# Kernel optimization log

Hardware: AMD Instinct MI355X
Metric: run time of the kernel (lower is better)

## Reference

```python
import jax, jax.numpy as jnp
import numpy as np

B, S, H = 2, 2048, 2048
NH, NKV, D = 16, 4, 128
E, K, F = 16, 2, 768
EPS = 1e-6
THETA = 1e6


def setup_inputs() -> dict:
    key = jax.random.key(0)
    ks = jax.random.split(key, 10)
    sd = 0.02
    rn = lambda k, shp: jax.random.normal(k, shp, jnp.float32) * sd
    return {
        "positions": jnp.arange(S, dtype=jnp.int32),
        "hidden_states": jax.random.normal(ks[0], (B, S, H), jnp.float32),
        "residual": jax.random.normal(ks[1], (B, S, H), jnp.float32),
        "w_in_ln": jnp.ones((H,), jnp.float32),
        "wq": rn(ks[2], (H, NH * D)),
        "wk": rn(ks[3], (H, NKV * D)),
        "wv": rn(ks[4], (H, NKV * D)),
        "wo": rn(ks[5], (NH * D, H)),
        "q_norm_w": jnp.ones((D,), jnp.float32),
        "k_norm_w": jnp.ones((D,), jnp.float32),
        "w_post_ln": jnp.ones((H,), jnp.float32),
        "gate_w": rn(ks[6], (H, E)),
        "w_gate_up": rn(ks[7], (E, H, 2 * F)),
        "w_down": rn(ks[8], (E, F, H)),
    }


def _rmsnorm(x, w):
    return x * jax.lax.rsqrt(jnp.mean(x * x, axis=-1, keepdims=True) + EPS) * w


def _rope(x, positions):
    # x: [B, S, h, D], neox-style rotate-half RoPE
    half = D // 2
    inv_freq = 1.0 / (THETA ** (jnp.arange(half, dtype=jnp.float32) / half))
    ang = positions.astype(jnp.float32)[:, None] * inv_freq  # [S, half]
    cos = jnp.cos(ang)[None, :, None, :]
    sin = jnp.sin(ang)[None, :, None, :]
    x1, x2 = x[..., :half], x[..., half:]
    return jnp.concatenate([x1 * cos - x2 * sin, x2 * cos + x1 * sin], axis=-1)


def reference(positions, hidden_states, residual, w_in_ln, wq, wk, wv, wo,
              q_norm_w, k_norm_w, w_post_ln, gate_w, w_gate_up, w_down):
    # fused RMSNorm + residual (residual is not None branch)
    residual = hidden_states + residual
    h = _rmsnorm(residual, w_in_ln)

    # --- Qwen3 attention: qk-norm + RoPE + causal GQA ---
    q = _rmsnorm((h @ wq).reshape(B, S, NH, D), q_norm_w)
    k = _rmsnorm((h @ wk).reshape(B, S, NKV, D), k_norm_w)
    v = (h @ wv).reshape(B, S, NKV, D)
    q = _rope(q, positions)
    k = _rope(k, positions)
    rep = NH // NKV
    k = jnp.repeat(k, rep, axis=2)
    v = jnp.repeat(v, rep, axis=2)
    scores = jnp.einsum('bqhd,bkhd->bhqk', q, k) / np.sqrt(D).astype(np.float32)
    causal = jnp.tril(jnp.ones((S, S), bool))
    scores = jnp.where(causal, scores, -jnp.inf)
    attn = jax.nn.softmax(scores, axis=-1)
    o = jnp.einsum('bhqk,bkhd->bqhd', attn, v).reshape(B, S, NH * D) @ wo

    # fused RMSNorm + residual
    residual = o + residual
    h = _rmsnorm(residual, w_post_ln)

    # --- MoE: top-k router (renormalized) + capacity-based grouped GEMM dispatch ---
    x = h.reshape(-1, H)                      # [T, H]
    T = B * S
    probs = jax.nn.softmax((x @ gate_w).astype(jnp.float32), axis=-1)
    tw, tids = jax.lax.top_k(probs, K)        # [T, K]
    tw = (tw / tw.sum(axis=-1, keepdims=True)).astype(x.dtype)

    P = T * K
    C = (2 * P) // E
    eids = tids.reshape(-1)                   # [P]
    oneh = jax.nn.one_hot(eids, E, dtype=jnp.int32)
    pos_in_e = (jnp.cumsum(oneh, axis=0) * oneh).sum(-1) - 1   # slot within expert
    valid = pos_in_e < C
    pos_c = jnp.minimum(pos_in_e, C - 1)
    e_safe = jnp.where(valid, eids, E)        # overflow -> dump row E

    xr = jnp.repeat(x, K, axis=0)             # [P, H]
    buf = jnp.zeros((E + 1, C, H), x.dtype).at[e_safe, pos_c].set(xr)[:E]
    gu = jnp.einsum('ech,ehf->ecf', buf, w_gate_up)            # [E, C, 2F]
    g, u = jnp.split(gu, 2, axis=-1)
    dn = jnp.einsum('ecf,efh->ech', jax.nn.silu(g) * u, w_down)
    dn = jnp.concatenate([dn, jnp.zeros((1, C, H), dn.dtype)], axis=0)
    yp = dn[e_safe, pos_c] * tw.reshape(-1)[:, None]           # [P, H]
    y = yp.reshape(T, K, H).sum(axis=1)
    return y.reshape(B, S, H), residual
```

## Files before the change

kernel.cpp:

```cpp
#include <hip/hip_runtime.h>
#include <stdint.h>

#define T_TOK 4096
#define HDIM  2048
#define SEQ   2048
#define NHQ   16
#define NKVH  4
#define DH    128
#define NE    16
#define CCAP  1024
#define FF    768
#define EPSF  1e-6f

typedef __attribute__((ext_vector_type(4))) float          f32x4;
typedef __attribute__((ext_vector_type(8))) _Float16       f16x8;
typedef __attribute__((ext_vector_type(4))) unsigned short u16x4;
typedef __attribute__((ext_vector_type(8))) unsigned short u16x8;

__device__ __forceinline__ unsigned short f2h(float f){ return __builtin_bit_cast(unsigned short, (_Float16)f); }
__device__ __forceinline__ float h2f(unsigned short u){ return (float)__builtin_bit_cast(_Float16, u); }
__device__ __forceinline__ void split2(float x, unsigned short& hi, unsigned short& lo){
  unsigned short h = f2h(x);
  hi = h; lo = f2h((x - h2f(h)) * 4096.f);
}
__device__ __forceinline__ void gl_lds16(const void* g, void* l){
  __builtin_amdgcn_global_load_lds((const __attribute__((address_space(1))) unsigned int*)g,
                                   (__attribute__((address_space(3))) unsigned int*)l, 16, 0, 0);
}
__device__ __forceinline__ int bswz(int row){ return ((row & 7) ^ ((row >> 3) & 7)) << 3; }

__global__ __launch_bounds__(256) void k_addnorm(
    const float* __restrict__ hs, const float* __restrict__ rs, const float* __restrict__ w,
    float* __restrict__ resid, unsigned short* __restrict__ hhi, unsigned short* __restrict__ hlo)
{
  int t = blockIdx.x, tid = threadIdx.x;
  size_t off = (size_t)t * HDIM;
  float4 a0 = ((const float4*)(hs+off))[tid];
  float4 b0 = ((const float4*)(rs+off))[tid];
  float4 a1 = ((const float4*)(hs+off))[tid+256];
  float4 b1 = ((const float4*)(rs+off))[tid+256];
  float4 s0 = make_float4(a0.x+b0.x, a0.y+b0.y, a0.z+b0.z, a0.w+b0.w);
  float4 s1 = make_float4(a1.x+b1.x, a1.y+b1.y, a1.z+b1.z, a1.w+b1.w);
  float ssq = s0.x*s0.x+s0.y*s0.y+s0.z*s0.z+s0.w*s0.w
            + s1.x*s1.x+s1.y*s1.y+s1.z*s1.z+s1.w*s1.w;
  #pragma unroll
  for (int sh=1; sh<64; sh<<=1) ssq += __shfl_xor(ssq, sh);
  __shared__ float red[4];
  if ((tid & 63) == 0) red[tid>>6] = ssq;
  __syncthreads();
  float tot = red[0]+red[1]+red[2]+red[3];
  float r = 1.f / sqrtf(tot * (1.f/HDIM) + EPSF);
  ((float4*)(resid+off))[tid]     = s0;
  ((float4*)(resid+off))[tid+256] = s1;
  float4 w0 = ((const float4*)w)[tid];
  float4 w1 = ((const float4*)w)[tid+256];
  u16x4 hv, lv; unsigned short ta, tb;
  split2(s0.x*r*w0.x, ta, tb); hv.x=ta; lv.x=tb;
  split2(s0.y*r*w0.y, ta, tb); hv.y=ta; lv.y=tb;
  split2(s0.z*r*w0.z, ta, tb); hv.z=ta; lv.z=tb;
  split2(s0.w*r*w0.w, ta, tb); hv.w=ta; lv.w=tb;
  ((u16x4*)(hhi+off))[tid] = hv; ((u16x4*)(hlo+off))[tid] = lv;
  split2(s1.x*r*w1.x, ta, tb); hv.x=ta; lv.x=tb;
  split2(s1.y*r*w1.y, ta, tb); hv.y=ta; lv.y=tb;
  split2(s1.z*r*w1.z, ta, tb); hv.z=ta; lv.z=tb;
  split2(s1.w*r*w1.w, ta, tb); hv.w=ta; lv.w=tb;
  ((u16x4*)(hhi+off))[tid+256] = hv; ((u16x4*)(hlo+off))[tid+256] = lv;
}

__global__ void k_cstab(const int* __restrict__ pos, float* __restrict__ cs)
{
  int i = blockIdx.x*256 + threadIdx.x;
  if (i >= SEQ*64) return;
  int s = i >> 6, f = i & 63;
  float pw  = (float)exp((double)f * 13.815510557964274 / 64.0);
  float inv = 1.0f / pw;
  float ang = (float)pos[s] * inv;
  float sv, cv;
  sincosf(ang, &sv, &cv);
  ((float2*)cs)[i] = make_float2(cv, sv);
}

__global__ __launch_bounds__(256) void k_normrope(
    unsigned short* __restrict__ qh, unsigned short* __restrict__ ql,
    unsigned short* __restrict__ kh, unsigned short* __restrict__ kl,
    const float* __restrict__ qnw, const float* __restrict__ knw,
    const float* __restrict__ cs)
{
  int t = blockIdx.x, head = blockIdx.y*4 + (threadIdx.x>>6), lane = threadIdx.x & 63;
  int s = t & (SEQ-1);
  unsigned short *dh, *dl; const float* wn; float scale; size_t off;
  if (head < NHQ){ off = ((size_t)t*NHQ + head)*DH; dh = qh+off; dl = ql+off; wn = qnw; scale = 0.08838834764831845f; }
  else           { off = ((size_t)t*NKVH + (head-NHQ))*DH; dh = kh+off; dl = kl+off; wn = knw; scale = 1.f; }
  float x1 = h2f(dh[lane])    + h2f(dl[lane])   *(1.f/4096.f);
  float x2 = h2f(dh[lane+64]) + h2f(dl[lane+64])*(1.f/4096.f);
  float ssq = x1*x1 + x2*x2;
  #pragma unroll
  for (int sh=1; sh<64; sh<<=1) ssq += __shfl_xor(ssq, sh);
  float r = 1.f / sqrtf(ssq * (1.f/DH) + EPSF);
  float y1 = x1*r*wn[lane], y2 = x2*r*wn[lane+64];
  float2 csp = ((const float2*)cs)[s*64 + lane];
  float o1 = (y1*csp.x - y2*csp.y) * scale;
  float o2 = (y2*csp.x + y1*csp.y) * scale;
  unsigned short a, b;
  split2(o1, a, b); dh[lane]    = a; dl[lane]    = b;
  split2(o2, a, b); dh[lane+64] = a; dl[lane+64] = b;
}

__global__ __launch_bounds__(256) void k_wsplit(
    const float* __restrict__ W, int Kd, int Ncols,
    unsigned short* __restrict__ Whi, unsigned short* __restrict__ Wlo)
{
  int k0 = blockIdx.x*64, n0 = blockIdx.y*64;
  __shared__ float T[64][65];
  int tid = threadIdx.x;
  int tr = tid >> 4;
  int tc = (tid & 15) * 4;
  #pragma unroll
  for (int i=0;i<4;i++){
    int k = tr + i*16;
    float4 v = *(const float4*)(W + (size_t)(k0 + k)*Ncols + n0 + tc);
    T[k][tc+0]=v.x; T[k][tc+1]=v.y; T[k][tc+2]=v.z; T[k][tc+3]=v.w;
  }
  __syncthreads();
  int n  = tid >> 2;
  int kc = (tid & 3) * 16;
  u16x8 hv0, lv0, hv1, lv1;
  #pragma unroll
  for (int j=0;j<8;j++){
    unsigned short hi, lo; split2(T[kc+j][n], hi, lo);
    hv0[j]=hi; lv0[j]=lo;
  }
  #pragma unroll
  for (int j=0;j<8;j++){
    unsigned short hi, lo; split2(T[kc+8+j][n], hi, lo);
    hv1[j]=hi; lv1[j]=lo;
  }
  size_t ob = (size_t)(n0 + n)*Kd + k0 + kc;
  *(u16x8*)(Whi + ob)     = hv0;
  *(u16x8*)(Whi + ob + 8) = hv1;
  *(u16x8*)(Wlo + ob)     = lv0;
  *(u16x8*)(Wlo + ob + 8) = lv1;
}

__global__ __launch_bounds__(256,2) void k_gemm_qkv(
    const unsigned short* __restrict__ Ahi, const unsigned short* __restrict__ Alo,
    const unsigned short* __restrict__ Whi, const unsigned short* __restrict__ Wlo,
    unsigned short* __restrict__ qh, unsigned short* __restrict__ ql,
    unsigned short* __restrict__ kh, unsigned short* __restrict__ kl,
    unsigned short* __restrict__ vh, unsigned short* __restrict__ vl)
{
  const int Kd = HDIM;
  int bm = blockIdx.x, bn2 = blockIdx.y;
  int bn, N, noff; unsigned short *Ch, *Cl;
  if (bn2 < 16){ bn = bn2;      N = 2048; noff = 0;    Ch = qh; Cl = ql; }
  else if (bn2 < 20){ bn = bn2-16; N = 512; noff = 2048; Ch = kh; Cl = kl; }
  else { bn = bn2-20; N = 512; noff = 2560; Ch = vh; Cl = vl; }

  __shared__ unsigned short As[2][8192];
  __shared__ unsigned short Bs[2][8192];

  int tid = threadIdx.x, lane = tid & 63, w = tid >> 6;
  int wr = w >> 1, wc = w & 1;

  size_t arow_g[4], brow_g[4];
  int lb_[4];
  #pragma unroll
  for (int i=0;i<4;i++){
    int ob = w*4096 + i*1024 + lane*16;
    int row = ob >> 7;
    int colB = ob & 127;
    int scolB = colB ^ ((row & 7) << 4);
    arow_g[i] = (size_t)(bm*128 + row) * Kd + (scolB >> 1);
    brow_g[i] = (size_t)(noff + bn*128 + row) * Kd + (scolB >> 1);
    lb_[i] = (w*4096 + i*1024) >> 1;
  }

  f32x4 accA[4][4] = {};
  f32x4 accB[4][4] = {};

  for (int kt = 0; kt < Kd/64; kt++){
    #pragma unroll
    for (int i=0;i<4;i++){
      gl_lds16(Ahi + arow_g[i] + kt*64, (void*)&As[0][lb_[i]]);
      gl_lds16(Alo + arow_g[i] + kt*64, (void*)&As[1][lb_[i]]);
      gl_lds16(Whi + brow_g[i] + kt*64, (void*)&Bs[0][lb_[i]]);
      gl_lds16(Wlo + brow_g[i] + kt*64, (void*)&Bs[1][lb_[i]]);
    }
    __syncthreads();
    #pragma unroll
    for (int kk=0; kk<2; kk++){
      f16x8 ah[4], al[4], bh[4], bl[4];
      #pragma unroll
      for (int m=0;m<4;m++){
        int row = wr*64 + m*16 + (lane & 15);
        int ci = (kk*32 + ((lane>>4)<<3)) ^ ((row & 7) << 3);
        ah[m] = *(const f16x8*)&As[0][row*64 + ci];
        al[m] = *(const f16x8*)&As[1][row*64 + ci];
      }
      #pragma unroll
      for (int n=0;n<4;n++){
        int row = wc*64 + n*16 + (lane & 15);
        int ci = (kk*32 + ((lane>>4)<<3)) ^ ((row & 7) << 3);
        bh[n] = *(const f16x8*)&Bs[0][row*64 + ci];
        bl[n] = *(const f16x8*)&Bs[1][row*64 + ci];
      }
      #pragma unroll
      for (int m=0;m<4;m++)
        #pragma unroll
        for (int n=0;n<4;n++){
          accA[m][n] = __builtin_amdgcn_mfma_f32_16x16x32_f16(ah[m], bh[n], accA[m][n], 0,0,0);
          accB[m][n] = __builtin_amdgcn_mfma_f32_16x16x32_f16(ah[m], bl[n], accB[m][n], 0,0,0);
          accB[m][n] = __builtin_amdgcn_mfma_f32_16x16x32_f16(al[m], bh[n], accB[m][n], 0,0,0);
        }
    }
    __syncthreads();
  }
  int r0 = (lane >> 4) << 2, c0 = lane & 15;
  #pragma unroll
  for (int m=0;m<4;m++){
    int grow0 = bm*128 + wr*64 + m*16 + r0;
    #pragma unroll
    for (int n=0;n<4;n++){
      int gcol = bn*128 + wc*64 + n*16 + c0;
      #pragma unroll
      for (int j=0;j<4;j++){
        float v = accA[m][n][j] + accB[m][n][j] * (1.f/4096.f);
        int grow = grow0 + j;
        unsigned short hi, lo; split2(v, hi, lo);
        Ch[(size_t)grow*N + gcol] = hi;
        Cl[(size_t)grow*N + gcol] = lo;
      }
    }
  }
}

template<int MODE>
__global__ __launch_bounds__(256,2) void k_gemm(
    const unsigned short* __restrict__ Ahi, const unsigned short* __restrict__ Alo,
    const float* __restrict__ Bsrc,
    const unsigned short* __restrict__ Bhi, const unsigned short* __restrict__ Blo,
    void* __restrict__ C1,
    int N, int Kd,
    const int* __restrict__ erow, const int* __restrict__ counts,
    const float* __restrict__ topw)
{
  constexpr int SPLIT = (MODE <= 2) ? 1 : 0;
  int bm = blockIdx.x, bn = blockIdx.y, e = blockIdx.z;
  int cnt = 0;
  const unsigned short* Abase = Ahi;
  const float* Bp = Bsrc;
  if constexpr (MODE == 4){ cnt = counts[e]; if (bm*128 >= cnt) return; Bp = Bsrc + (size_t)e*Kd*N; Abase = Ahi + (size_t)e*CCAP*Kd; }

  __shared__ unsigned short As[SPLIT?2:1][8192];
  __shared__ unsigned short Bs[SPLIT?2:1][8192];

  int tid = threadIdx.x, lane = tid & 63, w = tid >> 6;
  int wr = w >> 1, wc = w & 1;

  size_t arow_g[4], brow_g[4];
  int lb_[4];
  #pragma unroll
  for (int i=0;i<4;i++){
    int ob = w*4096 + i*1024 + lane*16;
    int row = ob >> 7;
    int colB = ob & 127;
    int scolB = colB ^ ((row & 7) << 4);
    int grow = bm*128 + row;
    arow_g[i] = (size_t)grow * Kd + (scolB >> 1);
    brow_g[i] = (size_t)(bn*128 + row) * Kd + (scolB >> 1);
    lb_[i] = (w*4096 + i*1024) >> 1;
  }

  f32x4 accA[4][4] = {};
  f32x4 accB[4][4] = {};

  int nK = Kd >> 6;
  for (int kt = 0; kt < nK; kt++){
    #pragma unroll
    for (int i=0;i<4;i++){
      gl_lds16(Abase + arow_g[i] + kt*64, (void*)&As[0][lb_[i]]);
      if constexpr (SPLIT) gl_lds16(Alo + arow_g[i] + kt*64, (void*)&As[1][lb_[i]]);
    }
    if constexpr (SPLIT){
      #pragma unroll
      for (int i=0;i<4;i++){
        gl_lds16(Bhi + brow_g[i] + kt*64, (void*)&Bs[0][lb_[i]]);
        gl_lds16(Blo + brow_g[i] + kt*64, (void*)&Bs[1][lb_[i]]);
      }
    } else {
      #pragma unroll
      for (int it=0; it<2; it++){
        int b2 = tid + it*256;
        int k0 = (b2 >> 5) << 2;
        int n0 = (b2 & 31) << 2;
        const float* bp = Bp + (size_t)(kt*64 + k0)*N + bn*128 + n0;
        float4 f0 = *(const float4*)bp;
        float4 f1 = *(const float4*)(bp + (size_t)N);
        float4 f2 = *(const float4*)(bp + 2*(size_t)N);
        float4 f3 = *(const float4*)(bp + 3*(size_t)N);
        #define DO_COL(J, CX) { \
          int rown = n0 + J; \
          int idx = rown*64 + (k0 ^ bswz(rown)); \
          u16x4 ph; ph.x=f2h(f0.CX); ph.y=f2h(f1.CX); ph.z=f2h(f2.CX); ph.w=f2h(f3.CX); \
          *(u16x4*)&Bs[0][idx] = ph; }
        DO_COL(0, x) DO_COL(1, y) DO_COL(2, z) DO_COL(3, w)
        #undef DO_COL
      }
    }
    __syncthreads();
    #pragma unroll
    for (int kk=0; kk<2; kk++){
      f16x8 ah[4], al[4], bh[4], bl[4];
      #pragma unroll
      for (int m=0;m<4;m++){
        int row = wr*64 + m*16 + (lane & 15);
        int ci = (kk*32 + ((lane>>4)<<3)) ^ ((row & 7) << 3);
        ah[m] = *(const f16x8*)&As[0][row*64 + ci];
        if constexpr (SPLIT) al[m] = *(const f16x8*)&As[1][row*64 + ci];
      }
      #pragma unroll
      for (int n=0;n<4;n++){
        int row = wc*64 + n*16 + (lane & 15);
        int sw = SPLIT ? ((row & 7) << 3) : bswz(row);
        int ci = (kk*32 + ((lane>>4)<<3)) ^ sw;
        bh[n] = *(const f16x8*)&Bs[0][row*64 + ci];
        if constexpr (SPLIT) bl[n] = *(const f16x8*)&Bs[1][row*64 + ci];
      }
      #pragma unroll
      for (int m=0;m<4;m++)
        #pragma unroll
        for (int n=0;n<4;n++){
          accA[m][n] = __builtin_amdgcn_mfma_f32_16x16x32_f16(ah[m], bh[n], accA[m][n], 0,0,0);
          if constexpr (SPLIT){
            accB[m][n] = __builtin_amdgcn_mfma_f32_16x16x32_f16(ah[m], bl[n], accB[m][n], 0,0,0);
            accB[m][n] = __builtin_amdgcn_mfma_f32_16x16x32_f16(al[m], bh[n], accB[m][n], 0,0,0);
          }
        }
    }
    __syncthreads();
  }
  int r0 = (lane >> 4) << 2, c0 = lane & 15;
  #pragma unroll
  for (int m=0;m<4;m++){
    int grow0 = bm*128 + wr*64 + m*16 + r0;
    #pragma unroll
    for (int n=0;n<4;n++){
      int gcol = bn*128 + wc*64 + n*16 + c0;
      #pragma unroll
      for (int j=0;j<4;j++){
        float v = accA[m][n][j];
        if constexpr (SPLIT) v += accB[m][n][j] * (1.f/4096.f);
        int grow = grow0 + j;
        if constexpr (MODE == 2){
          size_t idx = (size_t)grow*N + gcol;
          ((float*)C1)[idx] += v;
        } else if constexpr (MODE == 4){
          if (grow < cnt){
            int p = erow[e*CCAP + grow];
            ((float*)C1)[(size_t)p*N + gcol] = v;
          }
        }
      }
    }
  }
}

__global__ __launch_bounds__(256,2) void k_gemm_gu(
    const unsigned short* __restrict__ Ahi,
    const float* __restrict__ Bsrc,
    unsigned short* __restrict__ act,
    const int* __restrict__ erow, const int* __restrict__ counts)
{
  const int Kd = HDIM, N = 1536;
  int bm = blockIdx.x, bn = blockIdx.y, e = blockIdx.z;
  int cnt = counts[e]; if (bm*128 >= cnt) return;
  const float* Bp = Bsrc + (size_t)e*Kd*N;

  __shared__ unsigned short As [8192];
  __shared__ unsigned short BsG[8192];
  __shared__ unsigned short BsU[8192];

  int tid = threadIdx.x, lane = tid & 63, w = tid >> 6;
  int wr = w >> 1, wc = w & 1;

  size_t arow_g[4];
  int lb_[4];
  #pragma unroll
  for (int i=0;i<4;i++){
    int ob = w*4096 + i*1024 + lane*16;
    int row = ob >> 7;
    int colB = ob & 127;
    int scolB = colB ^ ((row & 7) << 4);
    int grow = erow[e*CCAP + bm*128 + row] >> 1;
    arow_g[i] = (size_t)grow * Kd + (scolB >> 1);
    lb_[i] = (w*4096 + i*1024) >> 1;
  }

  f32x4 accG[4][4] = {};
  f32x4 accU[4][4] = {};

  for (int kt = 0; kt < Kd/64; kt++){
    #pragma unroll
    for (int i=0;i<4;i++)
      gl_lds16(Ahi + arow_g[i] + kt*64, (void*)&As[lb_[i]]);
    #pragma unroll
    for (int it=0; it<2; it++){
      int b2 = tid + it*256;
      int k0 = (b2 >> 5) << 2;
      int n0 = (b2 & 31) << 2;
      const float* bpg = Bp + (size_t)(kt*64 + k0)*N + bn*128 + n0;
      const float* bpu = bpg + 768;
      float4 g0 = *(const float4*)bpg;
      float4 g1 = *(const float4*)(bpg + (size_t)N);
      float4 g2 = *(const float4*)(bpg + 2*(size_t)N);
      float4 g3 = *(const float4*)(bpg + 3*(size_t)N);
      float4 u0 = *(const float4*)bpu;
      float4 u1 = *(const float4*)(bpu + (size_t)N);
      float4 u2 = *(const float4*)(bpu + 2*(size_t)N);
      float4 u3 = *(const float4*)(bpu + 3*(size_t)N);
      #define DO_COL2(J, CX) { \
        int rown = n0 + J; \
        int idx = rown*64 + (k0 ^ bswz(rown)); \
        u16x4 pg; pg.x=f2h(g0.CX); pg.y=f2h(g1.CX); pg.z=f2h(g2.CX); pg.w=f2h(g3.CX); \
        *(u16x4*)&BsG[idx] = pg; \
        u16x4 pu; pu.x=f2h(u0.CX); pu.y=f2h(u1.CX); pu.z=f2h(u2.CX); pu.w=f2h(u3.CX); \
        *(u16x4*)&BsU[idx] = pu; }
      DO_COL2(0, x) DO_COL2(1, y) DO_COL2(2, z) DO_COL2(3, w)
      #undef DO_COL2
    }
    __syncthreads();
    #pragma unroll
    for (int kk=0; kk<2; kk++){
      f16x8 ah[4], bg[4], bu[4];
      #pragma unroll
      for (int m=0;m<4;m++){
        int row = wr*64 + m*16 + (lane & 15);
        int ci = (kk*32 + ((lane>>4)<<3)) ^ ((row & 7) << 3);
        ah[m] = *(const f16x8*)&As[row*64 + ci];
      }
      #pragma unroll
      for (int n=0;n<4;n++){
        int row = wc*64 + n*16 + (lane & 15);
        int ci = (kk*32 + ((lane>>4)<<3)) ^ bswz(row);
        bg[n] = *(const f16x8*)&BsG[row*64 + ci];
        bu[n] = *(const f16x8*)&BsU[row*64 + ci];
      }
      #pragma unroll
      for (int m=0;m<4;m++)
        #pragma unroll
        for (int n=0;n<4;n++){
          accG[m][n] = __builtin_amdgcn_mfma_f32_16x16x32_f16(ah[m], bg[n], accG[m][n], 0,0,0);
          accU[m][n] = __builtin_amdgcn_mfma_f32_16x16x32_f16(ah[m], bu[n], accU[m][n], 0,0,0);
        }
    }
    __syncthreads();
  }
  int r0 = (lane >> 4) << 2, c0 = lane & 15;
  #pragma unroll
  for (int m=0;m<4;m++){
    int grow0 = bm*128 + wr*64 + m*16 + r0;
    #pragma unroll
    for (int n=0;n<4;n++){
      int gcol = bn*128 + wc*64 + n*16 + c0;
      #pragma unroll
      for (int j=0;j<4;j++){
        int grow = grow0 + j;
        unsigned short g16 = f2h(accG[m][n][j]);
        unsigned short u16_ = f2h(accU[m][n][j]);
        float gf = h2f(g16), uf = h2f(u16_);
        float s = gf / (1.f + __expf(-gf));
        act[((size_t)e*CCAP + grow)*FF + gcol] = f2h(s * uf);
      }
    }
  }
}

__global__ __launch_bounds__(512,2) void k_attn(
    const unsigned short* __restrict__ qh, const unsigned short* __restrict__ ql,
    const unsigned short* __restrict__ kh, const unsigned short* __restrict__ kl,
    const unsigned short* __restrict__ vh, const unsigned short* __restrict__ vl,
    unsigned short* __restrict__ oh, unsigned short* __restrict__ ol)
{
  int h = blockIdx.y, b = blockIdx.z;
  int qt = b ? (15 - blockIdx.x) : blockIdx.x;
  int hkv = h >> 2;
  int tid = threadIdx.x, lane = tid & 63, w = tid >> 6;

  __shared__ unsigned short Ks[2][2][8192];
  __shared__ unsigned short Vs[2][2][8192];
  __shared__ unsigned short Ps[8][2][1024];

  int qrow = qt*128 + w*16 + (lane & 15);
  size_t qoff = ((size_t)(b*SEQ + qrow)*NHQ + h)*DH + ((lane>>4)<<3);
  f16x8 qfh[4], qfl[4];
  #pragma unroll
  for (int kk=0; kk<4; kk++){
    qfh[kk] = *(const f16x8*)(qh + qoff + kk*32);
    qfl[kk] = *(const f16x8*)(ql + qoff + kk*32);
  }

  const size_t SROW = (size_t)NKVH*DH;
  size_t kvbase = (size_t)b*SEQ*SROW + (size_t)hkv*DH;
  int kob[2]; size_t koff[2];
  #pragma unroll
  for (int i=0;i<2;i++){
    int ob = i*8192 + tid*16;
    int row = ob >> 8;
    int scol = (ob & 255) ^ ((row & 7) << 4);
    kob[i] = ob;
    koff[i] = (size_t)row*SROW + (scol >> 1);
  }
  int vkvp = (tid & 31) * 2;
  int vd0  = ((tid >> 5) & 15) * 8;
  size_t voff0 = (size_t)vkvp*SROW + vd0;
  size_t voff1 = voff0 + SROW;

  u16x8 pkh[2], pkl[2];
  u16x8 pvh[2], pvl[2];

  #define STAGE_LOAD(KVT) { \
    size_t tb = kvbase + (size_t)(KVT)*64*SROW; \
    _Pragma("unroll") \
    for (int i=0;i<2;i++){ pkh[i] = *(const u16x8*)(kh + tb + koff[i]); \
                           pkl[i] = *(const u16x8*)(kl + tb + koff[i]); } \
    pvh[0] = *(const u16x8*)(vh + tb + voff0); \
    pvh[1] = *(const u16x8*)(vh + tb + voff1); \
    pvl[0] = *(const u16x8*)(vl + tb + voff0); \
    pvl[1] = *(const u16x8*)(vl + tb + voff1); }

  #define STAGE_WRITE_K(BUF) { \
    _Pragma("unroll") \
    for (int i=0;i<2;i++){ \
      *(u16x8*)((char*)&Ks[BUF][0][0] + kob[i]) = pkh[i]; \
      *(u16x8*)((char*)&Ks[BUF][1][0] + kob[i]) = pkl[i]; } }

  #define STAGE_WRITE_V(BUF) { \
    _Pragma("unroll") \
    for (int jj=0;jj<8;jj++){ \
      int row = vd0 + jj; \
      int idx = row*64 + (vkvp ^ ((jj & 7) << 3)); \
      *(unsigned int*)&Vs[BUF][0][idx] = (unsigned int)pvh[0][jj] | ((unsigned int)pvh[1][jj] << 16); \
      *(unsigned int*)&Vs[BUF][1][idx] = (unsigned int)pvl[0][jj] | ((unsigned int)pvl[1][jj] << 16); } }

  #define QKT(KVT, BUF) { \
    f32x4 saA[4] = {}; \
    f32x4 saB[4] = {}; \
    __builtin_amdgcn_s_setprio(1); \
    _Pragma("unroll") \
    for (int kk=0; kk<4; kk++){ \
      _Pragma("unroll") \
      for (int n=0;n<4;n++){ \
        int row = n*16 + (lane & 15); \
        int ci = (kk*32 + ((lane>>4)<<3)) ^ ((row & 7) << 3); \
        f16x8 kfh = *(const f16x8*)&Ks[BUF][0][row*128 + ci]; \
        f16x8 kfl = *(const f16x8*)&Ks[BUF][1][row*128 + ci]; \
        saA[n] = __builtin_amdgcn_mfma_f32_16x16x32_f16(qfh[kk], kfh, saA[n], 0,0,0); \
        saB[n] = __builtin_amdgcn_mfma_f32_16x16x32_f16(qfh[kk], kfl, saB[n], 0,0,0); \
        saB[n] = __builtin_amdgcn_mfma_f32_16x16x32_f16(qfl[kk], kfh, saB[n], 0,0,0); } } \
    __builtin_amdgcn_s_setprio(0); \
    _Pragma("unroll") \
    for (int j=0;j<4;j++) mx[j] = -1e30f; \
    int qg = qt*128 + w*16 + ((lane>>4)<<2); \
    _Pragma("unroll") \
    for (int n=0;n<4;n++){ \
      int kvcol = (KVT)*64 + n*16 + (lane & 15); \
      _Pragma("unroll") \
      for (int j=0;j<4;j++){ \
        float sv = saA[n][j] + saB[n][j]*(1.f/4096.f); \
        if (kvcol > qg + j) sv = -1e30f; \
        p[n][j] = sv; \
        mx[j] = fmaxf(mx[j], sv); } } }

  #define SOFTMAX() { \
    _Pragma("unroll") \
    for (int sh=1; sh<16; sh<<=1) \
      _Pragma("unroll") \
      for (int j=0;j<4;j++) mx[j] = fmaxf(mx[j], __shfl_xor(mx[j], sh)); \
    float rs[4], sum[4]; \
    _Pragma("unroll") \
    for (int j=0;j<4;j++){ \
      float mn = fmaxf(m_[j], mx[j]); \
      rs[j] = __expf(m_[j] - mn); \
      float sm = 0.f; \
      _Pragma("unroll") \
      for (int n=0;n<4;n++){ float pe = __expf(p[n][j] - mn); p[n][j] = pe; sm += pe; } \
      sum[j] = sm; \
      m_[j] = mn; } \
    _Pragma("unroll") \
    for (int sh=1; sh<16; sh<<=1) \
      _Pragma("unroll") \
      for (int j=0;j<4;j++) sum[j] += __shfl_xor(sum[j], sh); \
    _Pragma("unroll") \
    for (int j=0;j<4;j++) l_[j] = l_[j]*rs[j] + sum[j]; \
    _Pragma("unroll") \
    for (int d=0;d<8;d++) \
      _Pragma("unroll") \
      for (int j=0;j<4;j++){ oaccA[d][j] *= rs[j]; oaccB[d][j] *= rs[j]; } \
    _Pragma("unroll") \
    for (int n=0;n<4;n++) \
      _Pragma("unroll") \
      for (int j=0;j<4;j++){ \
        int r = ((lane>>4)<<2) + j; \
        int c = n*16 + (lane & 15); \
        int idx = r*64 + (c ^ ((r & 7) << 3)); \
        unsigned short ph, pl2; split2(p[n][j], ph, pl2); \
        Ps[w][0][idx] = ph; \
        Ps[w][1][idx] = pl2; } }

  #define PVOP(BUF) { \
    __builtin_amdgcn_s_setprio(1); \
    _Pragma("unroll") \
    for (int kk=0; kk<2; kk++){ \
      int prow = lane & 15; \
      int pidx = prow*64 + ((kk*32 + ((lane>>4)<<3)) ^ ((prow & 7) << 3)); \
      f16x8 pah = *(const f16x8*)&Ps[w][0][pidx]; \
      f16x8 pal = *(const f16x8*)&Ps[w][1][pidx]; \
      _Pragma("unroll") \
      for (int d=0;d<8;d++){ \
        int row = d*16 + (lane & 15); \
        int ci = (kk*32 + ((lane>>4)<<3)) ^ ((row & 7) << 3); \
        f16x8 vfh = *(const f16x8*)&Vs[BUF][0][row*64 + ci]; \
        f16x8 vfl = *(const f16x8*)&Vs[BUF][1][row*64 + ci]; \
        oaccA[d] = __builtin_amdgcn_mfma_f32_16x16x32_f16(pah, vfh, oaccA[d], 0,0,0); \
        oaccB[d] = __builtin_amdgcn_mfma_f32_16x16x32_f16(pah, vfl, oaccB[d], 0,0,0); \
        oaccB[d] = __builtin_amdgcn_mfma_f32_16x16x32_f16(pal, vfh, oaccB[d], 0,0,0); } } \
    __builtin_amdgcn_s_setprio(0); }

  float m_[4], l_[4];
  f32x4 oaccA[8] = {};
  f32x4 oaccB[8] = {};
  #pragma unroll
  for (int j=0;j<4;j++){ m_[j] = -1e30f; l_[j] = 0.f; }

  int nkt = 2*qt + 2;
  STAGE_LOAD(0); STAGE_WRITE_K(0); STAGE_WRITE_V(0);
  STAGE_LOAD(1); STAGE_WRITE_K(1); STAGE_WRITE_V(1);
  __syncthreads();

  float p[4][4], mx[4];
  QKT(0, 0);

  for (int kvt = 0; kvt < nkt; kvt++){
    int cur = kvt & 1, nxt = cur ^ 1;
    bool h2 = (kvt+2 < nkt);
    if (h2){
      STAGE_LOAD(kvt+2);
      if (kvt) STAGE_WRITE_K(cur);
    }
    bool active = (kvt*64 <= qt*128 + w*16 + 15);
    bool actn   = (kvt+1 < nkt) && ((kvt+1)*64 <= qt*128 + w*16 + 15);
    if (actn){
      SOFTMAX();
      QKT(kvt+1, nxt);
      PVOP(cur);
    } else if (active){
      SOFTMAX();
      PVOP(cur);
    }
    __syncthreads();
    if (h2){
      if (!kvt){ STAGE_WRITE_K(cur); __syncthreads(); }
      STAGE_WRITE_V(cur);
    }
  }
  #undef STAGE_LOAD
  #undef STAGE_WRITE_K
  #undef STAGE_WRITE_V
  #undef QKT
  #undef SOFTMAX
  #undef PVOP

  #pragma unroll
  for (int j=0;j<4;j++) l_[j] = 1.f / l_[j];
  #pragma unroll
  for (int d=0;d<8;d++)
    #pragma unroll
    for (int j=0;j<4;j++){
      int qr = qt*128 + w*16 + ((lane>>4)<<2) + j;
      size_t off = ((size_t)(b*SEQ + qr)*NHQ + h)*DH + d*16 + (lane & 15);
      float v = (oaccA[d][j] + oaccB[d][j]*(1.f/4096.f)) * l_[j];
      unsigned short hi, lo; split2(v, hi, lo);
      oh[off] = hi; ol[off] = lo;
    }
}

__global__ __launch_bounds__(256) void k_ln2gate(
    const float* __restrict__ resid, const float* __restrict__ wln,
    const float* __restrict__ gw,
    unsigned short* __restrict__ x2, float* __restrict__ topw, int* __restrict__ topid)
{
  int t = blockIdx.x, tid = threadIdx.x;
  size_t off = (size_t)t * HDIM;
  float4 s0 = ((const float4*)(resid+off))[tid];
  float4 s1 = ((const float4*)(resid+off))[tid+256];
  float ssq = s0.x*s0.x+s0.y*s0.y+s0.z*s0.z+s0.w*s0.w
            + s1.x*s1.x+s1.y*s1.y+s1.z*s1.z+s1.w*s1.w;
  #pragma unroll
  for (int sh=1; sh<64; sh<<=1) ssq += __shfl_xor(ssq, sh);
  __shared__ float red[4];
  if ((tid & 63) == 0) red[tid>>6] = ssq;
  __syncthreads();
  float tot = red[0]+red[1]+red[2]+red[3];
  float r = 1.f / sqrtf(tot * (1.f/HDIM) + EPSF);
  float4 w0 = ((const float4*)wln)[tid];
  float4 w1 = ((const float4*)wln)[tid+256];
  float xs[8] = { s0.x*r*w0.x, s0.y*r*w0.y, s0.z*r*w0.z, s0.w*r*w0.w,
                  s1.x*r*w1.x, s1.y*r*w1.y, s1.z*r*w1.z, s1.w*r*w1.w };
  u16x4 hv;
  hv.x = f2h(xs[0]); hv.y = f2h(xs[1]); hv.z = f2h(xs[2]); hv.w = f2h(xs[3]);
  ((u16x4*)(x2+off))[tid] = hv;
  hv.x = f2h(xs[4]); hv.y = f2h(xs[5]); hv.z = f2h(xs[6]); hv.w = f2h(xs[7]);
  ((u16x4*)(x2+off))[tid+256] = hv;

  double acc[16];
  #pragma unroll
  for (int e2=0;e2<16;e2++) acc[e2] = 0.0;
  #pragma unroll
  for (int i=0;i<8;i++){
    int hidx = (i<4) ? (tid*4 + i) : (1024 + tid*4 + (i-4));
    const float4* g4 = (const float4*)(gw + (size_t)hidx*NE);
    float4 ga=g4[0], gb=g4[1], gc=g4[2], gd=g4[3];
    double xx = (double)xs[i];
    acc[0]+=xx*ga.x;  acc[1]+=xx*ga.y;  acc[2]+=xx*ga.z;  acc[3]+=xx*ga.w;
    acc[4]+=xx*gb.x;  acc[5]+=xx*gb.y;  acc[6]+=xx*gb.z;  acc[7]+=xx*gb.w;
    acc[8]+=xx*gc.x;  acc[9]+=xx*gc.y;  acc[10]+=xx*gc.z; acc[11]+=xx*gc.w;
    acc[12]+=xx*gd.x; acc[13]+=xx*gd.y; acc[14]+=xx*gd.z; acc[15]+=xx*gd.w;
  }
  __shared__ double red2[256][16];
  #pragma unroll
  for (int e2=0;e2<16;e2++) red2[tid][e2] = acc[e2];
  __syncthreads();
  for (int s=128; s>=1; s>>=1){
    if (tid < s){
      #pragma unroll
      for (int e2=0;e2<16;e2++) red2[tid][e2] += red2[tid+s][e2];
    }
    __syncthreads();
  }
  if (tid == 0){
    float l[16];
    #pragma unroll
    for (int e2=0;e2<16;e2++) l[e2] = (float)red2[0][e2];
    int i0 = 0;
    #pragma unroll
    for (int e2=1;e2<16;e2++) if (l[e2] > l[i0]) i0 = e2;
    int i1 = (i0 == 0) ? 1 : 0;
    #pragma unroll
    for (int e2=0;e2<16;e2++) if (e2 != i0 && l[e2] > l[i1]) i1 = e2;
    float w0t = 1.f / (1.f + expf(l[i1] - l[i0]));
    topw[t*2+0] = w0t; topw[t*2+1] = 1.f - w0t;
    topid[t*2+0] = i0; topid[t*2+1] = i1;
  }
}

__global__ __launch_bounds__(256) void k_route(
    int* __restrict__ topid, int* __restrict__ erow, int* __restrict__ counts)
{
  int tid = threadIdx.x;
  __shared__ unsigned short cnt[256][16];
  for (int i = tid; i < NE*CCAP; i += 256) erow[i] = 0;
  int loc[16];
  #pragma unroll
  for (int e2=0;e2<16;e2++) loc[e2] = 0;
  int myid[32];
  for (int i=0;i<32;i++){
    int e2 = topid[tid*32 + i];
    myid[i] = e2;
    loc[e2]++;
  }
  #pragma unroll
  for (int e2=0;e2<16;e2++) cnt[tid][e2] = (unsigned short)loc[e2];
  __syncthreads();
  if (tid < 16){
    int run = 0;
    for (int i=0;i<256;i++){ int c = cnt[i][tid]; cnt[i][tid] = (unsigned short)run; run += c; }
    counts[tid] = run > CCAP ? CCAP : run;
  }
  __syncthreads();
  #pragma unroll
  for (int e2=0;e2<16;e2++) loc[e2] = cnt[tid][e2];
  for (int i=0;i<32;i++){
    int e2 = myid[i];
    int pos = loc[e2]++;
    int p = tid*32 + i;
    int ok = (pos < CCAP);
    if (ok) erow[e2*CCAP + pos] = p;
    topid[p] = ok;
  }
}

__global__ __launch_bounds__(256) void k_gather(
    const float* __restrict__ yp, const int* __restrict__ valid,
    const float* __restrict__ topw, float* __restrict__ y)
{
  int t = blockIdx.x, tid = threadIdx.x;
  int v0 = valid[t*2+0], v1 = valid[t*2+1];
  float w0 = topw[t*2+0], w1 = topw[t*2+1];
  size_t o = (size_t)t*2*HDIM;
  const float4* r0 = (const float4*)(yp + o);
  const float4* r1 = (const float4*)(yp + o + HDIM);
  float4* yo = (float4*)(y + (size_t)t*HDIM);
  #pragma unroll
  for (int i=0;i<2;i++){
    int ix = tid + i*256;
    float4 a = r0[ix];
    float4 b = r1[ix];
    float4 out;
    float a0 = v0 ? w0 : 0.f;
    float b0 = v1 ? w1 : 0.f;
    out.x = (v0 ? a.x*a0 : 0.f) + (v1 ? b.x*b0 : 0.f);
    out.y = (v0 ? a.y*a0 : 0.f) + (v1 ? b.y*b0 : 0.f);
    out.z = (v0 ? a.z*a0 : 0.f) + (v1 ? b.z*b0 : 0.f);
    out.w = (v0 ? a.w*a0 : 0.f) + (v1 ? b.w*b0 : 0.f);
    yo[ix] = out;
  }
}

extern "C" void kernel_launch(void* const* d_in, const int* in_sizes, int n_in,
                              void* d_out, int out_size, void* d_ws, size_t ws_size,
                              hipStream_t stream)
{
  (void)in_sizes; (void)n_in; (void)out_size; (void)ws_size;
  const int*   positions = (const int*)  d_in[0];
  const float* hs        = (const float*)d_in[1];
  const float* res       = (const float*)d_in[2];
  const float* w_in_ln   = (const float*)d_in[3];
  const float* wq        = (const float*)d_in[4];
  const float* wk        = (const float*)d_in[5];
  const float* wv        = (const float*)d_in[6];
  const float* wo        = (const float*)d_in[7];
  const float* q_norm_w  = (const float*)d_in[8];
  const float* k_norm_w  = (const float*)d_in[9];
  const float* w_post_ln = (const float*)d_in[10];
  const float* gate_w    = (const float*)d_in[11];
  const float* w_gate_up = (const float*)d_in[12];
  const float* w_down    = (const float*)d_in[13];

  float* y      = (float*)d_out;
  float* resid2 = y + (size_t)T_TOK*HDIM;

  char* ws = (char*)d_ws;
  unsigned short* hhi = (unsigned short*)(ws + 0);
  unsigned short* hlo = (unsigned short*)(ws + 16777216);
  unsigned short* qh  = (unsigned short*)(ws + 33554432);
  unsigned short* ql  = (unsigned short*)(ws + 50331648);
  unsigned short* kh  = (unsigned short*)(ws + 67108864);
  unsigned short* kl  = (unsigned short*)(ws + 71303168);
  unsigned short* vh  = (unsigned short*)(ws + 75497472);
  unsigned short* vl  = (unsigned short*)(ws + 79691776);
  unsigned short* oh  = (unsigned short*)(ws + 83886080);
  unsigned short* ol  = (unsigned short*)(ws + 100663296);
  unsigned short* x2  = (unsigned short*)(ws + 117440512);
  unsigned short* qkvwh = (unsigned short*)(ws + 83886080);
  unsigned short* qkvwl = (unsigned short*)(ws + 96468992);
  unsigned short* wowh  = (unsigned short*)(ws + 117440512);
  unsigned short* wowl  = (unsigned short*)(ws + 125829120);
  unsigned short* act = (unsigned short*)(ws + 67108864);
  float*          yp  = (float*)         (ws + 0);
  float* cstab        = (float*)(ws + 134217728);
  float* topw         = (float*)(ws + 135266304);
  int*   topid        = (int*)  (ws + 135299072);
  int*   counts       = (int*)  (ws + 135331840);
  int*   erow         = (int*)  (ws + 135332096);

  k_addnorm<<<T_TOK, 256, 0, stream>>>(hs, res, w_in_ln, resid2, hhi, hlo);
  k_cstab<<<(SEQ*64 + 255)/256, 256, 0, stream>>>(positions, cstab);
  k_wsplit<<<dim3(32, 32), 256, 0, stream>>>(wq, HDIM, 2048, qkvwh,                     qkvwl);
  k_wsplit<<<dim3(32,  8), 256, 0, stream>>>(wk, HDIM,  512, qkvwh + (size_t)2048*HDIM, qkvwl + (size_t)2048*HDIM);
  k_wsplit<<<dim3(32,  8), 256, 0, stream>>>(wv, HDIM,  512, qkvwh + (size_t)2560*HDIM, qkvwl + (size_t)2560*HDIM);
  k_wsplit<<<dim3(32, 32), 256, 0, stream>>>(wo, HDIM, 2048, wowh,                      wowl);
  k_gemm_qkv<<<dim3(32,24,1), 256, 0, stream>>>(hhi, hlo, qkvwh, qkvwl, qh, ql, kh, kl, vh, vl);
  k_normrope<<<dim3(T_TOK, 5), 256, 0, stream>>>(qh, ql, kh, kl, q_norm_w, k_norm_w, cstab);
  k_attn<<<dim3(16, 16, 2), 512, 0, stream>>>(qh, ql, kh, kl, vh, vl, oh, ol);
  k_gemm<2><<<dim3(32,16,1), 256, 0, stream>>>(oh, ol, nullptr, wowh, wowl, resid2, 2048, 2048, nullptr, nullptr, nullptr);
  k_ln2gate<<<T_TOK, 256, 0, stream>>>(resid2, w_post_ln, gate_w, x2, topw, topid);
  k_route<<<1, 256, 0, stream>>>(topid, erow, counts);
  k_gemm_gu<<<dim3(8,6,16), 256, 0, stream>>>(x2, w_gate_up, act, erow, counts);
  k_gemm<4><<<dim3(8,16,16), 256, 0, stream>>>(act, nullptr, w_down, nullptr, nullptr, yp, 2048, 768, erow, counts, nullptr);
  k_gather<<<T_TOK, 256, 0, stream>>>(yp, topid, topw, y);
}
```

Measured before the change: 1.050 ms.

## Double-buffer LDS tiles in QKV and O-projection GEMMs, simplify attention staging

The QKV GEMM and a new dedicated O-projection GEMM now prefetch the next K-tile into a second LDS buffer while MFMAs run on the current one, so global-to-LDS latency is hidden. This doubles shared memory per block to 64KB, which may reduce occupancy below the requested two blocks per CU. The templated k_gemm is split into k_gemm_o and k_gemm_down specialisations. The attention kernel's staged K/V writes are merged into a single write followed by an extra barrier per iteration, which removes the earlier K-write overlap.

```diff
diff --git a/kernel.cpp b/kernel.cpp
--- a/kernel.cpp
+++ b/kernel.cpp
@@ -156,8 +156,8 @@
   else if (bn2 < 20){ bn = bn2-16; N = 512; noff = 2048; Ch = kh; Cl = kl; }
   else { bn = bn2-20; N = 512; noff = 2560; Ch = vh; Cl = vl; }
 
-  __shared__ unsigned short As[2][8192];
-  __shared__ unsigned short Bs[2][8192];
+  __shared__ unsigned short As[2][2][8192];
+  __shared__ unsigned short Bs[2][2][8192];
 
   int tid = threadIdx.x, lane = tid & 63, w = tid >> 6;
   int wr = w >> 1, wc = w & 1;
@@ -178,15 +178,19 @@
   f32x4 accA[4][4] = {};
   f32x4 accB[4][4] = {};
 
+  #define LOADT(KT, BUF) { \
+    _Pragma("unroll") \
+    for (int i=0;i<4;i++){ \
+      gl_lds16(Ahi + arow_g[i] + (KT)*64, (void*)&As[BUF][0][lb_[i]]); \
+      gl_lds16(Alo + arow_g[i] + (KT)*64, (void*)&As[BUF][1][lb_[i]]); \
+      gl_lds16(Whi + brow_g[i] + (KT)*64, (void*)&Bs[BUF][0][lb_[i]]); \
+      gl_lds16(Wlo + brow_g[i] + (KT)*64, (void*)&Bs[BUF][1][lb_[i]]); } }
+
+  LOADT(0, 0);
+  __syncthreads();
   for (int kt = 0; kt < Kd/64; kt++){
-    #pragma unroll
-    for (int i=0;i<4;i++){
-      gl_lds16(Ahi + arow_g[i] + kt*64, (void*)&As[0][lb_[i]]);
-      gl_lds16(Alo + arow_g[i] + kt*64, (void*)&As[1][lb_[i]]);
-      gl_lds16(Whi + brow_g[i] + kt*64, (void*)&Bs[0][lb_[i]]);
-      gl_lds16(Wlo + brow_g[i] + kt*64, (void*)&Bs[1][lb_[i]]);
-    }
-    __syncthreads();
+    int cur = kt & 1, nxt = cur ^ 1;
+    if (kt+1 < Kd/64) LOADT(kt+1, nxt);
     #pragma unroll
     for (int kk=0; kk<2; kk++){
       f16x8 ah[4], al[4], bh[4], bl[4];
@@ -194,15 +198,15 @@
       for (int m=0;m<4;m++){
         int row = wr*64 + m*16 + (lane & 15);
         int ci = (kk*32 + ((lane>>4)<<3)) ^ ((row & 7) << 3);
-        ah[m] = *(const f16x8*)&As[0][row*64 + ci];
-        al[m] = *(const f16x8*)&As[1][row*64 + ci];
+        ah[m] = *(const f16x8*)&As[cur][0][row*64 + ci];
+        al[m] = *(const f16x8*)&As[cur][1][row*64 + ci];
       }
       #pragma unroll
       for (int n=0;n<4;n++){
         int row = wc*64 + n*16 + (lane & 15);
         int ci = (kk*32 + ((lane>>4)<<3)) ^ ((row & 7) << 3);
-        bh[n] = *(const f16x8*)&Bs[0][row*64 + ci];
-        bl[n] = *(const f16x8*)&Bs[1][row*64 + ci];
+        bh[n] = *(const f16x8*)&Bs[cur][0][row*64 + ci];
+        bl[n] = *(const f16x8*)&Bs[cur][1][row*64 + ci];
       }
       #pragma unroll
       for (int m=0;m<4;m++)
@@ -215,6 +219,7 @@
     }
     __syncthreads();
   }
+  #undef LOADT
   int r0 = (lane >> 4) << 2, c0 = lane & 15;
   #pragma unroll
   for (int m=0;m<4;m++){
@@ -234,30 +239,114 @@
   }
 }
 
-template<int MODE>
-__global__ __launch_bounds__(256,2) void k_gemm(
+__global__ __launch_bounds__(256,2) void k_gemm_o(
     const unsigned short* __restrict__ Ahi, const unsigned short* __restrict__ Alo,
-    const float* __restrict__ Bsrc,
     const unsigned short* __restrict__ Bhi, const unsigned short* __restrict__ Blo,
-    void* __restrict__ C1,
-    int N, int Kd,
-    const int* __restrict__ erow, const int* __restrict__ counts,
-    const float* __restrict__ topw)
-{
-  constexpr int SPLIT = (MODE <= 2) ? 1 : 0;
-  int bm = blockIdx.x, bn = blockIdx.y, e = blockIdx.z;
-  int cnt = 0;
-  const unsigned short* Abase = Ahi;
-  const float* Bp = Bsrc;
-  if constexpr (MODE == 4){ cnt = counts[e]; if (bm*128 >= cnt) return; Bp = Bsrc + (size_t)e*Kd*N; Abase = Ahi + (size_t)e*CCAP*Kd; }
-
-  __shared__ unsigned short As[SPLIT?2:1][8192];
-  __shared__ unsigned short Bs[SPLIT?2:1][8192];
+    float* __restrict__ C1)
+{
+  const int Kd = HDIM, N = 2048;
+  int bm = blockIdx.x, bn = blockIdx.y;
+
+  __shared__ unsigned short As[2][2][8192];
+  __shared__ unsigned short Bs[2][2][8192];
 
   int tid = threadIdx.x, lane = tid & 63, w = tid >> 6;
   int wr = w >> 1, wc = w & 1;
 
   size_t arow_g[4], brow_g[4];
+  int lb_[4];
+  #pragma unroll
+  for (int i=0;i<4;i++){
+    int ob = w*4096 + i*1024 + lane*16;
+    int row = ob >> 7;
+    int colB = ob & 127;
+    int scolB = colB ^ ((row & 7) << 4);
+    arow_g[i] = (size_t)(bm*128 + row) * Kd + (scolB >> 1);
+    brow_g[i] = (size_t)(bn*128 + row) * Kd + (scolB >> 1);
+    lb_[i] = (w*4096 + i*1024) >> 1;
+  }
+
+  f32x4 accA[4][4] = {};
+  f32x4 accB[4][4] = {};
+
+  #define LOADT(KT, BUF) { \
+    _Pragma("unroll") \
+    for (int i=0;i<4;i++){ \
+      gl_lds16(Ahi + arow_g[i] + (KT)*64, (void*)&As[BUF][0][lb_[i]]); \
+      gl_lds16(Alo + arow_g[i] + (KT)*64, (void*)&As[BUF][1][lb_[i]]); \
+      gl_lds16(Bhi + brow_g[i] + (KT)*64, (void*)&Bs[BUF][0][lb_[i]]); \
+      gl_lds16(Blo + brow_g[i] + (KT)*64, (void*)&Bs[BUF][1][lb_[i]]); } }
+
+  LOADT(0, 0);
+  __syncthreads();
+  for (int kt = 0; kt < Kd/64; kt++){
+    int cur = kt & 1, nxt = cur ^ 1;
+    if (kt+1 < Kd/64) LOADT(kt+1, nxt);
+    #pragma unroll
+    for (int kk=0; kk<2; kk++){
+      f16x8 ah[4], al[4], bh[4], bl[4];
+      #pragma unroll
+      for (int m=0;m<4;m++){
+        int row = wr*64 + m*16 + (lane & 15);
+        int ci = (kk*32 + ((lane>>4)<<3)) ^ ((row & 7) << 3);
+        ah[m] = *(const f16x8*)&As[cur][0][row*64 + ci];
+        al[m] = *(const f16x8*)&As[cur][1][row*64 + ci];
+      }
+      #pragma unroll
+      for (int n=0;n<4;n++){
+        int row = wc*64 + n*16 + (lane & 15);
+        int ci = (kk*32 + ((lane>>4)<<3)) ^ ((row & 7) << 3);
+        bh[n] = *(const f16x8*)&Bs[cur][0][row*64 + ci];
+        bl[n] = *(const f16x8*)&Bs[cur][1][row*64 + ci];
+      }
+      #pragma unroll
+      for (int m=0;m<4;m++)
+        #pragma unroll
+        for (int n=0;n<4;n++){
+          accA[m][n] = __builtin_amdgcn_mfma_f32_16x16x32_f16(ah[m], bh[n], accA[m][n], 0,0,0);
+          accB[m][n] = __builtin_amdgcn_mfma_f32_16x16x32_f16(ah[m], bl[n], accB[m][n], 0,0,0);
+          accB[m][n] = __builtin_amdgcn_mfma_f32_16x16x32_f16(al[m], bh[n], accB[m][n], 0,0,0);
+        }
+    }
+    __syncthreads();
+  }
+  #undef LOADT
+  int r0 = (lane >> 4) << 2, c0 = lane & 15;
+  #pragma unroll
+  for (int m=0;m<4;m++){
+    int grow0 = bm*128 + wr*64 + m*16 + r0;
+    #pragma unroll
+    for (int n=0;n<4;n++){
+      int gcol = bn*128 + wc*64 + n*16 + c0;
+      #pragma unroll
+      for (int j=0;j<4;j++){
+        float v = accA[m][n][j] + accB[m][n][j] * (1.f/4096.f);
+        int grow = grow0 + j;
+        C1[(size_t)grow*N + gcol] += v;
+      }
+    }
+  }
+}
+
+__global__ __launch_bounds__(256,2) void k_gemm_down(
+    const unsigned short* __restrict__ Aact,
+    const float* __restrict__ Bsrc,
+    float* __restrict__ yp,
+    const int* __restrict__ erow, const int* __restrict__ counts)
+{
+  const int Kd = FF, N = HDIM;
+  int bm = blockIdx.x, bn = blockIdx.y, e = blockIdx.z;
+  int cnt = counts[e]; if (bm*128 >= cnt) return;
+  const float* Bp = Bsrc + (size_t)e*Kd*N;
+  const unsigned short* Abase = Aact + (size_t)e*CCAP*Kd;
+
+  __shared__ unsigned short As[8192];
+  __shared__ unsigned short Bs[8192];
+
+  int tid = threadIdx.x, lane = tid & 63, w = tid >> 6;
+  int wr = w >> 1, wc = w & 1;
+
+  size_t arow_g[4];
   int lb_[4];
   #pragma unroll
   for (int i=0;i<4;i++){
@@ -267,75 +356,55 @@
     int scolB = colB ^ ((row & 7) << 4);
     int grow = bm*128 + row;
     arow_g[i] = (size_t)grow * Kd + (scolB >> 1);
-    brow_g[i] = (size_t)(bn*128 + row) * Kd + (scolB >> 1);
     lb_[i] = (w*4096 + i*1024) >> 1;
   }
 
   f32x4 accA[4][4] = {};
-  f32x4 accB[4][4] = {};
 
   int nK = Kd >> 6;
   for (int kt = 0; kt < nK; kt++){
     #pragma unroll
-    for (int i=0;i<4;i++){
-      gl_lds16(Abase + arow_g[i] + kt*64, (void*)&As[0][lb_[i]]);
-      if constexpr (SPLIT) gl_lds16(Alo + arow_g[i] + kt*64, (void*)&As[1][lb_[i]]);
-    }
-    if constexpr (SPLIT){
-      #pragma unroll
-      for (int i=0;i<4;i++){
-        gl_lds16(Bhi + brow_g[i] + kt*64, (void*)&Bs[0][lb_[i]]);
-        gl_lds16(Blo + brow_g[i] + kt*64, (void*)&Bs[1][lb_[i]]);
-      }
-    } else {
-      #pragma unroll
-      for (int it=0; it<2; it++){
-        int b2 = tid + it*256;
-        int k0 = (b2 >> 5) << 2;
-        int n0 = (b2 & 31) << 2;
-        const float* bp = Bp + (size_t)(kt*64 + k0)*N + bn*128 + n0;
-        float4 f0 = *(const float4*)bp;
-        float4 f1 = *(const float4*)(bp + (size_t)N);
-        float4 f2 = *(const float4*)(bp + 2*(size_t)N);
-        float4 f3 = *(const float4*)(bp + 3*(size_t)N);
-        #define DO_COL(J, CX) { \
-          int rown = n0 + J; \
-          int idx = rown*64 + (k0 ^ bswz(rown)); \
-          u16x4 ph; ph.x=f2h(f0.CX); ph.y=f2h(f1.CX); ph.z=f2h(f2.CX); ph.w=f2h(f3.CX); \
-          *(u16x4*)&Bs[0][idx] = ph; }
-        DO_COL(0, x) DO_COL(1, y) DO_COL(2, z) DO_COL(3, w)
-        #undef DO_COL
-      }
+    for (int i=0;i<4;i++)
+      gl_lds16(Abase + arow_g[i] + kt*64, (void*)&As[lb_[i]]);
+    #pragma unroll
+    for (int it=0; it<2; it++){
+      int b2 = tid + it*256;
+      int k0 = (b2 >> 5) << 2;
+      int n0 = (b2 & 31) << 2;
+      const float* bp = Bp + (size_t)(kt*64 + k0)*N + bn*128 + n0;
+      float4 f0 = *(const float4*)bp;
+      float4 f1 = *(const float4*)(bp + (size_t)N);
+      float4 f2 = *(const float4*)(bp + 2*(size_t)N);
+      float4 f3 = *(const float4*)(bp + 3*(size_t)N);
+      #define DO_COL(J, CX) { \
+        int rown = n0 + J; \
+        int idx = rown*64 + (k0 ^ bswz(rown)); \
+        u16x4 ph; ph.x=f2h(f0.CX); ph.y=f2h(f1.CX); ph.z=f2h(f2.CX); ph.w=f2h(f3.CX); \
+        *(u16x4*)&Bs[idx] = ph; }
+      DO_COL(0, x) DO_COL(1, y) DO_COL(2, z) DO_COL(3, w)
+      #undef DO_COL
     }
     __syncthreads();
     #pragma unroll
     for (int kk=0; kk<2; kk++){
-      f16x8 ah[4], al[4], bh[4], bl[4];
+      f16x8 ah[4], bh[4];
       #pragma unroll
       for (int m=0;m<4;m++){
         int row = wr*64 + m*16 + (lane & 15);
         int ci = (kk*32 + ((lane>>4)<<3)) ^ ((row & 7) << 3);
-        ah[m] = *(const f16x8*)&As[0][row*64 + ci];
-        if constexpr (SPLIT) al[m] = *(const f16x8*)&As[1][row*64 + ci];
+        ah[m] = *(const f16x8*)&As[row*64 + ci];
       }
       #pragma unroll
       for (int n=0;n<4;n++){
         int row = wc*64 + n*16 + (lane & 15);
-        int sw = SPLIT ? ((row & 7) << 3) : bswz(row);
-        int ci = (kk*32 + ((lane>>4)<<3)) ^ sw;
-        bh[n] = *(const f16x8*)&Bs[0][row*64 + ci];
-        if constexpr (SPLIT) bl[n] = *(const f16x8*)&Bs[1][row*64 + ci];
+        int ci = (kk*32 + ((lane>>4)<<3)) ^ bswz(row);
+        bh[n] = *(const f16x8*)&Bs[row*64 + ci];
       }
       #pragma unroll
       for (int m=0;m<4;m++)
         #pragma unroll
-        for (int n=0;n<4;n++){
+        for (int n=0;n<4;n++)
           accA[m][n] = __builtin_amdgcn_mfma_f32_16x16x32_f16(ah[m], bh[n], accA[m][n], 0,0,0);
-          if constexpr (SPLIT){
-            accB[m][n] = __builtin_amdgcn_mfma_f32_16x16x32_f16(ah[m], bl[n], accB[m][n], 0,0,0);
-            accB[m][n] = __builtin_amdgcn_mfma_f32_16x16x32_f16(al[m], bh[n], accB[m][n], 0,0,0);
-          }
-        }
     }
     __syncthreads();
   }
@@ -348,17 +417,10 @@
       int gcol = bn*128 + wc*64 + n*16 + c0;
       #pragma unroll
       for (int j=0;j<4;j++){
-        float v = accA[m][n][j];
-        if constexpr (SPLIT) v += accB[m][n][j] * (1.f/4096.f);
         int grow = grow0 + j;
-        if constexpr (MODE == 2){
-          size_t idx = (size_t)grow*N + gcol;
-          ((float*)C1)[idx] += v;
-        } else if constexpr (MODE == 4){
-          if (grow < cnt){
-            int p = erow[e*CCAP + grow];
-            ((float*)C1)[(size_t)p*N + gcol] = v;
-          }
+        if (grow < cnt){
+          int p = erow[e*CCAP + grow];
+          yp[(size_t)p*N + gcol] = accA[m][n][j];
         }
       }
     }
@@ -528,13 +590,11 @@
     pvl[0] = *(const u16x8*)(vl + tb + voff0); \
     pvl[1] = *(const u16x8*)(vl + tb + voff1); }
 
-  #define STAGE_WRITE_K(BUF) { \
+  #define STAGE_WRITE(BUF) { \
     _Pragma("unroll") \
     for (int i=0;i<2;i++){ \
       *(u16x8*)((char*)&Ks[BUF][0][0] + kob[i]) = pkh[i]; \
-      *(u16x8*)((char*)&Ks[BUF][1][0] + kob[i]) = pkl[i]; } }
-
-  #define STAGE_WRITE_V(BUF) { \
+      *(u16x8*)((char*)&Ks[BUF][1][0] + kob[i]) = pkl[i]; } \
     _Pragma("unroll") \
     for (int jj=0;jj<8;jj++){ \
       int row = vd0 + jj; \
@@ -633,8 +693,8 @@
   for (int j=0;j<4;j++){ m_[j] = -1e30f; l_[j] = 0.f; }
 
   int nkt = 2*qt + 2;
-  STAGE_LOAD(0); STAGE_WRITE_K(0); STAGE_WRITE_V(0);
-  STAGE_LOAD(1); STAGE_WRITE_K(1); STAGE_WRITE_V(1);
+  STAGE_LOAD(0); STAGE_WRITE(0);
+  STAGE_LOAD(1); STAGE_WRITE(1);
   __syncthreads();
 
   float p[4][4], mx[4];
@@ -642,11 +702,8 @@
 
   for (int kvt = 0; kvt < nkt; kvt++){
     int cur = kvt & 1, nxt = cur ^ 1;
-    bool h2 = (kvt+2 < nkt);
-    if (h2){
-      STAGE_LOAD(kvt+2);
-      if (kvt) STAGE_WRITE_K(cur);
-    }
+    if (kvt+2 < nkt) STAGE_LOAD(kvt+2);
+
     bool active = (kvt*64 <= qt*128 + w*16 + 15);
     bool actn   = (kvt+1 < nkt) && ((kvt+1)*64 <= qt*128 + w*16 + 15);
     if (actn){
@@ -658,14 +715,11 @@
       PVOP(cur);
     }
     __syncthreads();
-    if (h2){
-      if (!kvt){ STAGE_WRITE_K(cur); __syncthreads(); }
-      STAGE_WRITE_V(cur);
-    }
+    if (kvt+2 < nkt) STAGE_WRITE(cur);
+    __syncthreads();
   }
   #undef STAGE_LOAD
-  #undef STAGE_WRITE_K
-  #undef STAGE_WRITE_V
+  #undef STAGE_WRITE
   #undef QKT
   #undef SOFTMAX
   #undef PVOP
@@ -872,10 +926,10 @@
   k_gemm_qkv<<<dim3(32,24,1), 256, 0, stream>>>(hhi, hlo, qkvwh, qkvwl, qh, ql, kh, kl, vh, vl);
   k_normrope<<<dim3(T_TOK, 5), 256, 0, stream>>>(qh, ql, kh, kl, q_norm_w, k_norm_w, cstab);
   k_attn<<<dim3(16, 16, 2), 512, 0, stream>>>(qh, ql, kh, kl, vh, vl, oh, ol);
-  k_gemm<2><<<dim3(32,16,1), 256, 0, stream>>>(oh, ol, nullptr, wowh, wowl, resid2, 2048, 2048, nullptr, nullptr, nullptr);
+  k_gemm_o<<<dim3(32,16,1), 256, 0, stream>>>(oh, ol, wowh, wowl, resid2);
   k_ln2gate<<<T_TOK, 256, 0, stream>>>(resid2, w_post_ln, gate_w, x2, topw, topid);
   k_route<<<1, 256, 0, stream>>>(topid, erow, counts);
   k_gemm_gu<<<dim3(8,6,16), 256, 0, stream>>>(x2, w_gate_up, act, erow, counts);
-  k_gemm<4><<<dim3(8,16,16), 256, 0, stream>>>(act, nullptr, w_down, nullptr, nullptr, yp, 2048, 768, erow, counts, nullptr);
+  k_gemm_down<<<dim3(8,16,16), 256, 0, stream>>>(act, w_down, yp, erow, counts);
   k_gather<<<T_TOK, 256, 0, stream>>>(yp, topid, topw, y);
 }
```

Measured after the change: 1.181 ms. +12.5%, slower.
